# Performance work log

Measured on AMD Instinct MI355X. Metric: run time of the kernel, lower is better.

Reference implementation:

```python
import jax, jax.numpy as jnp
import numpy as np

N_NODES = 100000
N_EDGES = 1600000
D_IN = 128
D_OUT = 128


def setup_inputs() -> dict:
    key = jax.random.key(0)
    k1, k2, k3, k4, k5 = jax.random.split(key, 5)
    feat = jax.random.normal(k1, (N_NODES, D_IN), dtype=jnp.float32)
    src = jax.random.randint(k2, (N_EDGES,), 0, N_NODES, dtype=jnp.int32)
    dst = jax.random.randint(k3, (N_EDGES,), 0, N_NODES, dtype=jnp.int32)
    # xavier-ish init for bias-free Linear weights, stored [out, in] like nn.Linear
    scale = float(np.sqrt(2.0 / (D_IN + D_OUT)))
    W_self = jax.random.normal(k4, (D_OUT, D_IN), dtype=jnp.float32) * scale
    W_neigh = jax.random.normal(k5, (D_OUT, D_IN), dtype=jnp.float32) * scale
    return {"feat": feat, "src": src, "dst": dst, "W_self": W_self, "W_neigh": W_neigh}


def reference(feat, src, dst, W_self, W_neigh):
    # SAGEConv, aggregator_type='mean':
    #   h_neigh = mean_{(u->v) in E} feat[u]   (per dst node v)
    #   out = feat @ W_self^T + h_neigh @ W_neigh^T
    n = feat.shape[0]
    msgs = feat[src]  # [E, D_in] gather (dominant memory traffic)
    summed = jax.ops.segment_sum(msgs, dst, num_segments=n)  # [N, D_in]
    deg = jax.ops.segment_sum(jnp.ones((src.shape[0],), feat.dtype), dst, num_segments=n)
    h_neigh = summed / jnp.maximum(deg, 1.0)[:, None]  # zero-degree -> 0 (DGL mean)
    return feat @ W_self.T + h_neigh @ W_neigh.T
```

## Files before the change

kernel.cpp:

```cpp
#include <hip/hip_runtime.h>
#include <hip/hip_bf16.h>

#define D 128
#define KDIM 256
#define BSHIFT 5
#define CPAD 16
#define MAX_BE 768
#define ROWS 32
#define LDK 264

#define NSCAT 250
#define CHUNK 6400
#define NBKT_CAP 3136

typedef __attribute__((ext_vector_type(8))) short short8;
typedef __attribute__((ext_vector_type(4))) float floatx4;

static __device__ __forceinline__ ushort f2bf(float x) {
    __hip_bfloat16 h = __float2bfloat16(x);
    return __builtin_bit_cast(ushort, h);
}

__global__ __launch_bounds__(512) void k_part_prep(
        const float* __restrict__ feat,
        const float* __restrict__ Wself,
        const float* __restrict__ Wneigh,
        const int* __restrict__ src,
        const int* __restrict__ dst,
        ushort* __restrict__ feat_b,
        ushort* __restrict__ Wc,
        int* __restrict__ gcur,
        uint* __restrict__ ep,
        int nb, int nbF, int nFeat8, int E) {
    __shared__ uint   sbuf[CHUNK];
    __shared__ ushort bbuf[CHUNK];
    __shared__ int    lhist[NBKT_CAP];
    __shared__ int    lbase[NBKT_CAP];

    const int blk = blockIdx.x;
    const int tid = threadIdx.x;

    if (blk < NSCAT) {
        for (int i = tid; i < NBKT_CAP; i += 512) lhist[i] = 0;
        __syncthreads();

        const int beg = blk * CHUNK;
        const int end = min(E, beg + CHUNK);
        const int cnt = end - beg;

        for (int i4 = beg / 4 + tid; i4 < end / 4; i4 += 512) {
            int4 s = ((const int4*)src)[i4];
            int4 d = ((const int4*)dst)[i4];
            int li = i4 * 4 - beg;
            sbuf[li + 0] = ((uint)s.x << BSHIFT) | (uint)(d.x & 31);
            sbuf[li + 1] = ((uint)s.y << BSHIFT) | (uint)(d.y & 31);
            sbuf[li + 2] = ((uint)s.z << BSHIFT) | (uint)(d.z & 31);
            sbuf[li + 3] = ((uint)s.w << BSHIFT) | (uint)(d.w & 31);
            int b0 = d.x >> BSHIFT, b1 = d.y >> BSHIFT;
            int b2 = d.z >> BSHIFT, b3 = d.w >> BSHIFT;
            bbuf[li + 0] = (ushort)b0;
            bbuf[li + 1] = (ushort)b1;
            bbuf[li + 2] = (ushort)b2;
            bbuf[li + 3] = (ushort)b3;
            atomicAdd(&lhist[b0], 1);
            atomicAdd(&lhist[b1], 1);
            atomicAdd(&lhist[b2], 1);
            atomicAdd(&lhist[b3], 1);
        }
        __syncthreads();

        for (int b2 = tid; b2 < nb; b2 += 512) {
            int c = lhist[b2];
            if (c) lbase[b2] = atomicAdd(&gcur[b2 * CPAD], c);
            lhist[b2] = 0;
        }
        __syncthreads();

        for (int i = tid; i < cnt; i += 512) {
            int b2 = bbuf[i];
            int off = atomicAdd(&lhist[b2], 1);
            int slot = lbase[b2] + off;
            if (slot < MAX_BE) ep[(size_t)b2 * MAX_BE + slot] = sbuf[i];
        }
    } else if (blk < NSCAT + nbF) {
        int i = (blk - NSCAT) * 512 + tid;
        if (i < nFeat8) {
            const float4* f4 = (const float4*)feat;
            float4 f0 = f4[(size_t)i * 2];
            float4 f1 = f4[(size_t)i * 2 + 1];
            ushort o[8];
            o[0] = f2bf(f0.x); o[1] = f2bf(f0.y);
            o[2] = f2bf(f0.z); o[3] = f2bf(f0.w);
            o[4] = f2bf(f1.x); o[5] = f2bf(f1.y);
            o[6] = f2bf(f1.z); o[7] = f2bf(f1.w);
            *(short8*)(feat_b + (size_t)i * 8) = *(short8*)o;
        }
    } else {
        int idx = (blk - NSCAT - nbF) * 512 + tid;
        if (idx < D * KDIM) {
            int j = idx >> 8;
            int k = idx & 255;
            float v = (k < D) ? Wself[j * D + k] : Wneigh[j * D + (k - D)];
            Wc[idx] = f2bf(v);
        }
    }
}

__global__ __launch_bounds__(256, 7) void sage_fused(
        const ushort* __restrict__ feat_b,
        const int* __restrict__ bcount,
        const uint* __restrict__ ep,
        const short* __restrict__ Wc,
        float* __restrict__ out,
        int N) {
    __shared__ ushort X[ROWS * LDK];
    __shared__ uint elist[MAX_BE];
    __shared__ int counts[32], offs[32], cur[32];

    const int tid = threadIdx.x;
    const int b = blockIdx.x;
    const int v0 = b * ROWS;

    const int e0 = b * MAX_BE;
    int cnt = min(bcount[b * CPAD], MAX_BE);

    if (tid < 32) { counts[tid] = 0; cur[tid] = 0; }

#pragma unroll
    for (int i = 0; i < 2; i++) {
        int idx = tid + i * 256;
        int r = idx >> 4;
        int c = idx & 15;
        int v = v0 + r;
        short8 f = {0, 0, 0, 0, 0, 0, 0, 0};
        if (v < N) f = *(const short8*)(feat_b + (size_t)v * D + c * 8);
        *(short8*)&X[r * LDK + c * 8] = f;
    }
    __syncthreads();

    for (int i = tid; i < cnt; i += 256) {
        uint p = ep[e0 + i];
        atomicAdd(&counts[p & 31], 1);
    }
    __syncthreads();
    if (tid == 0) {
        int run = 0;
#pragma unroll
        for (int i = 0; i < 32; i++) { offs[i] = run; run += counts[i]; }
    }
    __syncthreads();
    for (int i = tid; i < cnt; i += 256) {
        uint p = ep[e0 + i];
        int dl = p & 31;
        int slot = offs[dl] + atomicAdd(&cur[dl], 1);
        elist[slot] = p >> BSHIFT;
    }
    __syncthreads();

    {
        const int ln = tid >> 5;
        const int q = tid & 31;
        for (int g = 0; g < 4; g++) {
            int r = g * 8 + ln;
            int v = v0 + r;
            float4 acc = make_float4(0.f, 0.f, 0.f, 0.f);
            float rd = 0.f;
            if (v < N) {
                int dg = counts[r];
                int eb = offs[r];
                rd = (dg > 0) ? 1.0f / (float)dg : 0.f;
                int e = 0;
                for (; e + 7 < dg; e += 8) {
                    uint2 p[8];
#pragma unroll
                    for (int j = 0; j < 8; j++) {
                        uint u = elist[eb + e + j];
                        p[j] = *(const uint2*)(feat_b + (size_t)u * D + q * 4);
                    }
#pragma unroll
                    for (int j = 0; j < 8; j++) {
                        acc.x += __uint_as_float(p[j].x << 16);
                        acc.y += __uint_as_float(p[j].x & 0xffff0000u);
                        acc.z += __uint_as_float(p[j].y << 16);
                        acc.w += __uint_as_float(p[j].y & 0xffff0000u);
                    }
                }
                for (; e + 1 < dg; e += 2) {
                    uint ua = elist[eb + e], ub = elist[eb + e + 1];
                    uint2 pa = *(const uint2*)(feat_b + (size_t)ua * D + q * 4);
                    uint2 pb = *(const uint2*)(feat_b + (size_t)ub * D + q * 4);
                    acc.x += __uint_as_float(pa.x << 16) + __uint_as_float(pb.x << 16);
                    acc.y += __uint_as_float(pa.x & 0xffff0000u) + __uint_as_float(pb.x & 0xffff0000u);
                    acc.z += __uint_as_float(pa.y << 16) + __uint_as_float(pb.y << 16);
                    acc.w += __uint_as_float(pa.y & 0xffff0000u) + __uint_as_float(pb.y & 0xffff0000u);
                }
                if (e < dg) {
                    uint u = elist[eb + e];
                    uint2 pa = *(const uint2*)(feat_b + (size_t)u * D + q * 4);
                    acc.x += __uint_as_float(pa.x << 16);
                    acc.y += __uint_as_float(pa.x & 0xffff0000u);
                    acc.z += __uint_as_float(pa.y << 16);
                    acc.w += __uint_as_float(pa.y & 0xffff0000u);
                }
            }
            ushort o[4];
            o[0] = f2bf(acc.x * rd);
            o[1] = f2bf(acc.y * rd);
            o[2] = f2bf(acc.z * rd);
            o[3] = f2bf(acc.w * rd);
            *(ushort2*)&X[r * LDK + D + q * 4] = *(ushort2*)&o[0];
            *(ushort2*)&X[r * LDK + D + q * 4 + 2] = *(ushort2*)&o[2];
        }
    }
    __syncthreads();

    const int lane = tid & 63;
    const int w = tid >> 6;
    const int col = lane & 15;
    const int quad = lane >> 4;
    const int rowBase = (w & 1) * 16;
    const int ctBase = (w >> 1) * 4;

    floatx4 o[4];
#pragma unroll
    for (int ct = 0; ct < 4; ct++) o[ct] = (floatx4){0.f, 0.f, 0.f, 0.f};

#pragma unroll
    for (int kt = 0; kt < 8; kt++) {
        int k0 = kt * 32;
        short8 a = *(const short8*)&X[(rowBase + col) * LDK + k0 + quad * 8];
#pragma unroll
        for (int ct = 0; ct < 4; ct++) {
            short8 bfr = *(const short8*)(Wc + ((ctBase + ct) * 16 + col) * KDIM + k0 + quad * 8);
            o[ct] = __builtin_amdgcn_mfma_f32_16x16x32_bf16(a, bfr, o[ct], 0, 0, 0);
        }
    }

    int vbase = v0 + rowBase + quad * 4;
#pragma unroll
    for (int ct = 0; ct < 4; ct++) {
#pragma unroll
        for (int r = 0; r < 4; r++) {
            int v = vbase + r;
            if (v < N) out[(size_t)v * D + (ctBase + ct) * 16 + col] = o[ct][r];
        }
    }
}

extern "C" void kernel_launch(void* const* d_in, const int* in_sizes, int n_in,
                              void* d_out, int out_size, void* d_ws, size_t ws_size,
                              hipStream_t stream) {
    const float* feat   = (const float*)d_in[0];
    const int*   src    = (const int*)d_in[1];
    const int*   dst    = (const int*)d_in[2];
    const float* Wself  = (const float*)d_in[3];
    const float* Wneigh = (const float*)d_in[4];
    float* out = (float*)d_out;

    const int N = in_sizes[0] / D;
    const int E = in_sizes[1];
    const int nb = (N + ROWS - 1) / ROWS;

    char* ws = (char*)d_ws;
    size_t off = 0;
    auto carve = [&](size_t bytes) {
        char* p = ws + off;
        off = (off + bytes + 255) & ~(size_t)255;
        return p;
    };
    int*    gcur   = (int*)   carve((size_t)nb * CPAD * sizeof(int));
    uint*   ep     = (uint*)  carve((size_t)nb * MAX_BE * sizeof(uint));
    ushort* feat_b = (ushort*)carve((size_t)N * D * sizeof(ushort));
    ushort* Wc     = (ushort*)carve((size_t)D * KDIM * sizeof(ushort));

    const int nFeat8 = N * D / 8;
    const int nbF = (nFeat8 + 511) / 512;
    const int nbW = (D * KDIM + 511) / 512;

    (void)hipMemsetAsync(gcur, 0, (size_t)nb * CPAD * sizeof(int), stream);

    k_part_prep<<<NSCAT + nbF + nbW, 512, 0, stream>>>(
        feat, Wself, Wneigh, src, dst, feat_b, Wc, gcur, ep,
        nb, nbF, nFeat8, E);

    sage_fused<<<nb, 256, 0, stream>>>(feat_b, gcur, ep, (const short*)Wc, out, N);
}
```

Before: 241.7 us.

## Drop LDS edge staging in partition scatter and use fewer, larger chunks

The bucket-partition phase no longer stages packed edges and bucket ids in shared memory. It reads dst once to build the histogram, then rereads src and dst from global memory to scatter. The scatter block count drops from 250 to 64 and chunk size is now computed at runtime. This frees LDS so more blocks can be resident and cuts the number of global atomics on the bucket cursors. In exchange each scatter block does more serial work, dst is read twice, and fewer blocks are available to hide latency.

```diff
diff --git a/kernel.cpp b/kernel.cpp
--- a/kernel.cpp
+++ b/kernel.cpp
@@ -9,8 +9,7 @@
 #define ROWS 32
 #define LDK 264
 
-#define NSCAT 250
-#define CHUNK 6400
+#define NSCAT 64
 #define NBKT_CAP 3136
 
 typedef __attribute__((ext_vector_type(8))) short short8;
@@ -31,11 +30,9 @@
         ushort* __restrict__ Wc,
         int* __restrict__ gcur,
         uint* __restrict__ ep,
-        int nb, int nbF, int nFeat8, int E) {
-    __shared__ uint   sbuf[CHUNK];
-    __shared__ ushort bbuf[CHUNK];
-    __shared__ int    lhist[NBKT_CAP];
-    __shared__ int    lbase[NBKT_CAP];
+        int nb, int nbF, int nFeat8, int E, int chunk) {
+    __shared__ int lhist[NBKT_CAP];
+    __shared__ int lbase[NBKT_CAP];
 
     const int blk = blockIdx.x;
     const int tid = threadIdx.x;
@@ -44,43 +41,51 @@
         for (int i = tid; i < NBKT_CAP; i += 512) lhist[i] = 0;
         __syncthreads();
 
-        const int beg = blk * CHUNK;
-        const int end = min(E, beg + CHUNK);
-        const int cnt = end - beg;
-
-        for (int i4 = beg / 4 + tid; i4 < end / 4; i4 += 512) {
+        const int beg = blk * chunk;
+        const int end = min(E, beg + chunk);
+        const int beg4 = beg >> 2;
+        const int end4 = end >> 2;
+
+        for (int i4 = beg4 + tid; i4 < end4; i4 += 512) {
+            int4 d = ((const int4*)dst)[i4];
+            atomicAdd(&lhist[d.x >> BSHIFT], 1);
+            atomicAdd(&lhist[d.y >> BSHIFT], 1);
+            atomicAdd(&lhist[d.z >> BSHIFT], 1);
+            atomicAdd(&lhist[d.w >> BSHIFT], 1);
+        }
+        __syncthreads();
+
+        for (int b2 = tid; b2 < nb; b2 += 512) {
+            int c = lhist[b2];
+            lbase[b2] = c ? atomicAdd(&gcur[b2 * CPAD], c) : 0;
+            lhist[b2] = 0;
+        }
+        __syncthreads();
+
+        for (int i4 = beg4 + tid; i4 < end4; i4 += 512) {
             int4 s = ((const int4*)src)[i4];
             int4 d = ((const int4*)dst)[i4];
-            int li = i4 * 4 - beg;
-            sbuf[li + 0] = ((uint)s.x << BSHIFT) | (uint)(d.x & 31);
-            sbuf[li + 1] = ((uint)s.y << BSHIFT) | (uint)(d.y & 31);
-            sbuf[li + 2] = ((uint)s.z << BSHIFT) | (uint)(d.z & 31);
-            sbuf[li + 3] = ((uint)s.w << BSHIFT) | (uint)(d.w & 31);
-            int b0 = d.x >> BSHIFT, b1 = d.y >> BSHIFT;
-            int b2 = d.z >> BSHIFT, b3 = d.w >> BSHIFT;
-            bbuf[li + 0] = (ushort)b0;
-            bbuf[li + 1] = (ushort)b1;
-            bbuf[li + 2] = (ushort)b2;
-            bbuf[li + 3] = (ushort)b3;
-            atomicAdd(&lhist[b0], 1);
-            atomicAdd(&lhist[b1], 1);
-            atomicAdd(&lhist[b2], 1);
-            atomicAdd(&lhist[b3], 1);
-        }
-        __syncthreads();
-
-        for (int b2 = tid; b2 < nb; b2 += 512) {
-            int c = lhist[b2];
-            if (c) lbase[b2] = atomicAdd(&gcur[b2 * CPAD], c);
-            lhist[b2] = 0;
-        }
-        __syncthreads();
-
-        for (int i = tid; i < cnt; i += 512) {
-            int b2 = bbuf[i];
-            int off = atomicAdd(&lhist[b2], 1);
-            int slot = lbase[b2] + off;
-            if (slot < MAX_BE) ep[(size_t)b2 * MAX_BE + slot] = sbuf[i];
+            int b0, off, slot;
+            b0 = d.x >> BSHIFT;
+            off = atomicAdd(&lhist[b0], 1);
+            slot = lbase[b0] + off;
+            if (slot < MAX_BE)
+                ep[(size_t)b0 * MAX_BE + slot] = ((uint)s.x << BSHIFT) | (uint)(d.x & 31);
+            b0 = d.y >> BSHIFT;
+            off = atomicAdd(&lhist[b0], 1);
+            slot = lbase[b0] + off;
+            if (slot < MAX_BE)
+                ep[(size_t)b0 * MAX_BE + slot] = ((uint)s.y << BSHIFT) | (uint)(d.y & 31);
+            b0 = d.z >> BSHIFT;
+            off = atomicAdd(&lhist[b0], 1);
+            slot = lbase[b0] + off;
+            if (slot < MAX_BE)
+                ep[(size_t)b0 * MAX_BE + slot] = ((uint)s.z << BSHIFT) | (uint)(d.z & 31);
+            b0 = d.w >> BSHIFT;
+            off = atomicAdd(&lhist[b0], 1);
+            slot = lbase[b0] + off;
+            if (slot < MAX_BE)
+                ep[(size_t)b0 * MAX_BE + slot] = ((uint)s.w << BSHIFT) | (uint)(d.w & 31);
         }
     } else if (blk < NSCAT + nbF) {
         int i = (blk - NSCAT) * 512 + tid;
@@ -276,12 +281,13 @@
     const int nFeat8 = N * D / 8;
     const int nbF = (nFeat8 + 511) / 512;
     const int nbW = (D * KDIM + 511) / 512;
+    const int chunk = (((E + NSCAT - 1) / NSCAT) + 3) & ~3;
 
     (void)hipMemsetAsync(gcur, 0, (size_t)nb * CPAD * sizeof(int), stream);
 
     k_part_prep<<<NSCAT + nbF + nbW, 512, 0, stream>>>(
         feat, Wself, Wneigh, src, dst, feat_b, Wc, gcur, ep,
-        nb, nbF, nFeat8, E);
+        nb, nbF, nFeat8, E, chunk);
 
     sage_fused<<<nb, 256, 0, stream>>>(feat_b, gcur, ep, (const short*)Wc, out, N);
 }
```

After: 258.1 us. +6.8%, slower.
